# Performance work log

Measured on AMD Instinct MI355X. Metric: run time of the kernel, lower is better.

Reference implementation:

```python
import jax, jax.numpy as jnp
import numpy as np

# irreps '64x0e+32x1o+16x2e' as (mul, ir_dim, is_scalar)
IRREPS = [(64, 1, True), (32, 3, False), (16, 5, False)]
DIM = sum(m * d for m, d, _ in IRREPS)          # 240
NUM_FEATURES = sum(m for m, _, _ in IRREPS)      # 112
NUM_SCALAR = sum(m for m, _, s in IRREPS if s)   # 64
NUM_TYPE = 10
EPS = 1e-5
BATCH = 200000


def setup_inputs() -> dict:
    key = jax.random.key(0)
    k1, k2 = jax.random.split(key)
    x = jax.random.normal(k1, (BATCH, DIM), dtype=jnp.float32)
    input_type = jax.random.randint(k2, (BATCH,), 0, NUM_TYPE)
    weight = jnp.ones((NUM_TYPE, NUM_FEATURES), dtype=jnp.float32)
    bias = jnp.zeros((NUM_TYPE, NUM_SCALAR), dtype=jnp.float32)
    return {"x": x, "input_type": input_type, "weight": weight, "bias": bias}


def _type_mean(vals, input_type, counts):
    # scatter_mean over the batch dim into NUM_TYPE slots
    s = jax.ops.segment_sum(vals, input_type, num_segments=NUM_TYPE)
    return s / counts[:, None]


def reference(x, input_type, weight, bias):
    batch, dim = x.shape
    xr = x.reshape(batch, 1, dim)  # middle dim (no extra ... dims here)
    counts = jnp.maximum(
        jax.ops.segment_sum(jnp.ones((batch,), x.dtype), input_type, num_segments=NUM_TYPE),
        1.0,
    )
    fields = []
    ix = iw = ib = 0
    for mul, d, is_scalar in IRREPS:
        field = xr[:, :, ix:ix + mul * d].reshape(batch, -1, mul, d)
        ix += mul * d
        if is_scalar:
            fm = field.mean(1).reshape(batch, mul)                 # (batch, mul)
            fm = _type_mean(fm, input_type, counts)                # (num_type, mul)
            field = field - fm[input_type][:, None, :, None]
        # normalization='component': mean over ir dim; reduce='mean' over middle dim
        fn = jnp.square(field).mean(3).mean(1)                     # (batch, mul)
        fn = _type_mean(fn, input_type, counts)                    # (num_type, mul)
        fn = jax.lax.rsqrt(fn + EPS)
        fn = fn * weight[:, iw:iw + mul]
        iw += mul
        field = field * fn[input_type][:, None, :, None]
        if is_scalar:
            field = field + bias[:, ib:ib + mul][input_type][:, None, :, None]
            ib += mul
        fields.append(field.reshape(batch, -1, mul * d))
    out = jnp.concatenate(fields, axis=2)
    return out.reshape(batch, dim)
```

## Files before the change

### kernel.cpp

```cpp
#include <hip/hip_runtime.h>

#define DIM 240
#define NTYPE 10
#define NFEAT 112
#define NSLOT 176
#define NRED  1770
#define PSTRIDE 1792
#define RCHUNK 32
#define SROWS 16
#define EPSV 1e-5f

typedef float nf4 __attribute__((ext_vector_type(4)));


__global__ __launch_bounds__(256) void stats_kernel(const float* __restrict__ x,
        const int* __restrict__ type, float* __restrict__ partial, int B, int nblk)
{
    const int tid = threadIdx.x;
    const bool active = tid < DIM;
    const bool isScalar = tid < 64;

    float accA[NTYPE], accB[NTYPE];
#pragma unroll
    for (int t = 0; t < NTYPE; t++) { accA[t] = 0.f; accB[t] = 0.f; }

    const float inactAdd = (tid == 255) ? 1.f : 0.f;

    auto accum = [&](int ty, float v) {
        const float v2 = v * v;
        const float addA = active ? (isScalar ? v : v2) : inactAdd;
#pragma unroll
        for (int t = 0; t < NTYPE; t++) {
            if (t == ty) { accA[t] += addA; accB[t] += v2; }
        }
    };

    const int stride = nblk * SROWS;
    for (int row0 = blockIdx.x * SROWS; row0 + (SROWS - 1) < B; row0 += stride) {
        int ty[SROWS];
#pragma unroll
        for (int j = 0; j < SROWS; j++) ty[j] = type[row0 + j];
        float v[SROWS];
#pragma unroll
        for (int j = 0; j < SROWS; j++) v[j] = 0.f;
        if (active) {
            const float* p = x + (size_t)row0 * DIM + tid;
#pragma unroll
            for (int j = 0; j < SROWS; j++) v[j] = p[j * DIM];
        }
#pragma unroll
        for (int j = 0; j < SROWS; j++) accum(ty[j], v[j]);
    }
    if (blockIdx.x == 0) {
        for (int r = B & ~(SROWS - 1); r < B; r++) {
            const int ty0 = type[r];
            float v = active ? x[(size_t)r * DIM + tid] : 0.f;
            accum(ty0, v);
        }
    }

    __shared__ float sAcc[NRED];
    for (int i = tid; i < NRED; i += 256) sAcc[i] = 0.f;
    __syncthreads();

    if (isScalar) {
#pragma unroll
        for (int t = 0; t < NTYPE; t++) {
            sAcc[t * NSLOT + tid] = accA[t];
            sAcc[t * NSLOT + 64 + tid] = accB[t];
        }
    } else if (tid < 160) {
        const int ch = (tid - 64) / 3;
#pragma unroll
        for (int t = 0; t < NTYPE; t++)
            atomicAdd(&sAcc[t * NSLOT + 128 + ch], accA[t]);
    } else if (tid < DIM) {
        const int ch = (tid - 160) / 5;
#pragma unroll
        for (int t = 0; t < NTYPE; t++)
            atomicAdd(&sAcc[t * NSLOT + 160 + ch], accA[t]);
    } else if (tid == 255) {
#pragma unroll
        for (int t = 0; t < NTYPE; t++)
            sAcc[NTYPE * NSLOT + t] = accA[t];
    }
    __syncthreads();

    float* __restrict__ dst = partial + (size_t)blockIdx.x * PSTRIDE;
    for (int i = tid; i < NRED; i += 256) dst[i] = sAcc[i];
}

__global__ __launch_bounds__(256) void reduce1_kernel(const float* __restrict__ partial,
        float* __restrict__ gpart, int nblk)
{
    const int colChunk = blockIdx.x % 7;
    const int rowChunk = blockIdx.x / 7;
    const int col = colChunk * 256 + threadIdx.x;
    const int r0 = (rowChunk * nblk) / RCHUNK;
    const int r1 = ((rowChunk + 1) * nblk) / RCHUNK;
    float acc = 0.f;
#pragma unroll 8
    for (int r = r0; r < r1; r++)
        acc += partial[(size_t)r * PSTRIDE + col];
    gpart[rowChunk * PSTRIDE + col] = acc;
}

__global__ __launch_bounds__(256) void finalize_kernel(const float* __restrict__ gpart,
        const float* __restrict__ weight, const float* __restrict__ bias,
        float* __restrict__ params)
{
    const int t = blockIdx.x;
    const int c = threadIdx.x;

    __shared__ float scnt;
    if (c == 0) {
        float cs = 0.f;
#pragma unroll
        for (int k = 0; k < RCHUNK; k++)
            cs += gpart[k * PSTRIDE + NTYPE * NSLOT + t];
        scnt = fmaxf(cs, 1.f);
    }
    __syncthreads();
    if (c >= DIM) return;
    const float inv = 1.f / scnt;

    float sub = 0.f, mul, bia = 0.f;
    if (c < 64) {
        float S = 0.f, Q = 0.f;
#pragma unroll
        for (int k = 0; k < RCHUNK; k++) {
            const float* p = gpart + k * PSTRIDE + t * NSLOT;
            S += p[c]; Q += p[64 + c];
        }
        const float mean = S * inv;
        float var = Q * inv - mean * mean;
        var = fmaxf(var, 0.f);
        mul = rsqrtf(var + EPSV) * weight[t * NFEAT + c];
        sub = mean;
        bia = bias[t * 64 + c];
    } else if (c < 160) {
        const int ch = (c - 64) / 3;
        float N = 0.f;
#pragma unroll
        for (int k = 0; k < RCHUNK; k++)
            N += gpart[k * PSTRIDE + t * NSLOT + 128 + ch];
        mul = rsqrtf(N * inv * (1.f / 3.f) + EPSV) * weight[t * NFEAT + 64 + ch];
    } else {
        const int ch = (c - 160) / 5;
        float N = 0.f;
#pragma unroll
        for (int k = 0; k < RCHUNK; k++)
            N += gpart[k * PSTRIDE + t * NSLOT + 160 + ch];
        mul = rsqrtf(N * inv * 0.2f + EPSV) * weight[t * NFEAT + 96 + ch];
    }
    float* p = params + t * 720;
    p[c] = sub;
    p[240 + c] = mul;
    p[480 + c] = bia;
}

__global__ __launch_bounds__(256) void apply_kernel(const float* __restrict__ x,
        const int* __restrict__ type, const float* __restrict__ params,
        float* __restrict__ out, int B, int nblocks)
{
    __shared__ nf4 sp[NTYPE * 180];
    const int tid = threadIdx.x;
    const nf4* __restrict__ pg = (const nf4*)params;
    for (int i = tid; i < NTYPE * 180; i += 256) sp[i] = pg[i];
    __syncthreads();

    const int total = B * 60;
    const nf4* __restrict__ xv = (const nf4*)x;
    nf4* __restrict__ ov = (nf4*)out;
    const int estride = nblocks * 256;

    for (int base = blockIdx.x * 256 + tid; base < total; base += estride * 4) {
        int e0 = base, e1 = base + estride, e2 = base + 2 * estride, e3 = base + 3 * estride;
        const bool a0 = e0 < total, a1 = e1 < total, a2 = e2 < total, a3 = e3 < total;
        const int r0 = (int)(((unsigned long long)(unsigned)e0 * 2290649225ull) >> 37);
        const int r1 = a1 ? (int)(((unsigned long long)(unsigned)e1 * 2290649225ull) >> 37) : 0;
        const int r2 = a2 ? (int)(((unsigned long long)(unsigned)e2 * 2290649225ull) >> 37) : 0;
        const int r3 = a3 ? (int)(((unsigned long long)(unsigned)e3 * 2290649225ull) >> 37) : 0;
        const int c0 = e0 - r0 * 60, c1 = e1 - r1 * 60, c2 = e2 - r2 * 60, c3 = e3 - r3 * 60;
        int t0 = 0, t1 = 0, t2 = 0, t3 = 0;
        nf4 v0 = {0,0,0,0}, v1 = {0,0,0,0}, v2 = {0,0,0,0}, v3 = {0,0,0,0};
        if (a0) { t0 = type[r0]; v0 = xv[e0]; }
        if (a1) { t1 = type[r1]; v1 = xv[e1]; }
        if (a2) { t2 = type[r2]; v2 = xv[e2]; }
        if (a3) { t3 = type[r3]; v3 = xv[e3]; }
        if (a0) {
            const nf4 s = sp[t0 * 180 + c0];
            const nf4 m = sp[t0 * 180 + 60 + c0];
            const nf4 b = sp[t0 * 180 + 120 + c0];
            __builtin_nontemporal_store((v0 - s) * m + b, &ov[e0]);
        }
        if (a1) {
            const nf4 s = sp[t1 * 180 + c1];
            const nf4 m = sp[t1 * 180 + 60 + c1];
            const nf4 b = sp[t1 * 180 + 120 + c1];
            __builtin_nontemporal_store((v1 - s) * m + b, &ov[e1]);
        }
        if (a2) {
            const nf4 s = sp[t2 * 180 + c2];
            const nf4 m = sp[t2 * 180 + 60 + c2];
            const nf4 b = sp[t2 * 180 + 120 + c2];
            __builtin_nontemporal_store((v2 - s) * m + b, &ov[e2]);
        }
        if (a3) {
            const nf4 s = sp[t3 * 180 + c3];
            const nf4 m = sp[t3 * 180 + 60 + c3];
            const nf4 b = sp[t3 * 180 + 120 + c3];
            __builtin_nontemporal_store((v3 - s) * m + b, &ov[e3]);
        }
    }
}

extern "C" void kernel_launch(void* const* d_in, const int* in_sizes, int n_in,
                              void* d_out, int out_size, void* d_ws, size_t ws_size,
                              hipStream_t stream) {
    const float* x      = (const float*)d_in[0];
    const int*   type   = (const int*)d_in[1];
    const float* weight = (const float*)d_in[2];
    const float* bias   = (const float*)d_in[3];
    float* out = (float*)d_out;
    float* ws  = (float*)d_ws;
    const int B = in_sizes[0] / DIM;

    int nblk = 2048;
    size_t fixed = (size_t)RCHUNK * PSTRIDE + 7200;
    size_t need_floats = (size_t)nblk * PSTRIDE + fixed;
    if (ws_size < need_floats * 4) {
        nblk = (int)((ws_size / 4 - fixed) / PSTRIDE);
        if (nblk < 1) nblk = 1;
    }
    float* partial = ws;
    float* gpart   = ws + (size_t)nblk * PSTRIDE;
    float* params  = gpart + (size_t)RCHUNK * PSTRIDE;

    hipLaunchKernelGGL(stats_kernel, dim3(nblk), dim3(256), 0, stream,
                       x, type, partial, B, nblk);
    hipLaunchKernelGGL(reduce1_kernel, dim3(7 * RCHUNK), dim3(256), 0, stream,
                       partial, gpart, nblk);
    hipLaunchKernelGGL(finalize_kernel, dim3(NTYPE), dim3(256), 0, stream,
                       gpart, weight, bias, params);
    hipLaunchKernelGGL(apply_kernel, dim3(2048), dim3(256), 0, stream,
                       x, type, params, out, B, 2048);
}
```

Measured before the change: 379.9 us.

## Replace partial-sum reduction kernel with global atomics and compact apply params

The stats kernel now atomically adds each block's per-type sums into 32 striped global slots, zeroed by a memset beforehand. This removes the per-block partial buffer and the separate reduce1 kernel. The apply kernel's parameter table shrinks so that only the scalar channels load a mean and bias, while the other channels just multiply. In exchange, global atomics contend across 2048 blocks, a memset launch is added, and the summation order becomes nondeterministic.

```diff
diff --git a/kernel.cpp b/kernel.cpp
--- a/kernel.cpp
+++ b/kernel.cpp
@@ -8,13 +8,14 @@
 #define PSTRIDE 1792
 #define RCHUNK 32
 #define SROWS 16
+#define PT 384
 #define EPSV 1e-5f
 
 typedef float nf4 __attribute__((ext_vector_type(4)));
 
 
 __global__ __launch_bounds__(256) void stats_kernel(const float* __restrict__ x,
-        const int* __restrict__ type, float* __restrict__ partial, int B, int nblk)
+        const int* __restrict__ type, float* __restrict__ gpart, int B, int nblk)
 {
     const int tid = threadIdx.x;
     const bool active = tid < DIM;
@@ -86,23 +87,8 @@
     }
     __syncthreads();
 
-    float* __restrict__ dst = partial + (size_t)blockIdx.x * PSTRIDE;
-    for (int i = tid; i < NRED; i += 256) dst[i] = sAcc[i];
-}
-
-__global__ __launch_bounds__(256) void reduce1_kernel(const float* __restrict__ partial,
-        float* __restrict__ gpart, int nblk)
-{
-    const int colChunk = blockIdx.x % 7;
-    const int rowChunk = blockIdx.x / 7;
-    const int col = colChunk * 256 + threadIdx.x;
-    const int r0 = (rowChunk * nblk) / RCHUNK;
-    const int r1 = ((rowChunk + 1) * nblk) / RCHUNK;
-    float acc = 0.f;
-#pragma unroll 8
-    for (int r = r0; r < r1; r++)
-        acc += partial[(size_t)r * PSTRIDE + col];
-    gpart[rowChunk * PSTRIDE + col] = acc;
+    float* __restrict__ dst = gpart + (size_t)(blockIdx.x & (RCHUNK - 1)) * PSTRIDE;
+    for (int i = tid; i < NRED; i += 256) atomicAdd(&dst[i], sAcc[i]);
 }
 
 __global__ __launch_bounds__(256) void finalize_kernel(const float* __restrict__ gpart,
@@ -153,20 +139,19 @@
             N += gpart[k * PSTRIDE + t * NSLOT + 160 + ch];
         mul = rsqrtf(N * inv * 0.2f + EPSV) * weight[t * NFEAT + 96 + ch];
     }
-    float* p = params + t * 720;
-    p[c] = sub;
-    p[240 + c] = mul;
-    p[480 + c] = bia;
+    float* p = params + t * PT;
+    p[c] = mul;
+    if (c < 64) { p[240 + c] = sub; p[304 + c] = bia; }
 }
 
 __global__ __launch_bounds__(256) void apply_kernel(const float* __restrict__ x,
         const int* __restrict__ type, const float* __restrict__ params,
         float* __restrict__ out, int B, int nblocks)
 {
-    __shared__ nf4 sp[NTYPE * 180];
+    __shared__ nf4 sp[NTYPE * 96];
     const int tid = threadIdx.x;
     const nf4* __restrict__ pg = (const nf4*)params;
-    for (int i = tid; i < NTYPE * 180; i += 256) sp[i] = pg[i];
+    for (int i = tid; i < NTYPE * 96; i += 256) sp[i] = pg[i];
     __syncthreads();
 
     const int total = B * 60;
@@ -189,28 +174,28 @@
         if (a2) { t2 = type[r2]; v2 = xv[e2]; }
         if (a3) { t3 = type[r3]; v3 = xv[e3]; }
         if (a0) {
-            const nf4 s = sp[t0 * 180 + c0];
-            const nf4 m = sp[t0 * 180 + 60 + c0];
-            const nf4 b = sp[t0 * 180 + 120 + c0];
-            __builtin_nontemporal_store((v0 - s) * m + b, &ov[e0]);
+            const nf4 m = sp[t0 * 96 + c0];
+            nf4 o = v0 * m;
+            if (c0 < 16) o = (v0 - sp[t0 * 96 + 60 + c0]) * m + sp[t0 * 96 + 76 + c0];
+            __builtin_nontemporal_store(o, &ov[e0]);
         }
         if (a1) {
-            const nf4 s = sp[t1 * 180 + c1];
-            const nf4 m = sp[t1 * 180 + 60 + c1];
-            const nf4 b = sp[t1 * 180 + 120 + c1];
-            __builtin_nontemporal_store((v1 - s) * m + b, &ov[e1]);
+            const nf4 m = sp[t1 * 96 + c1];
+            nf4 o = v1 * m;
+            if (c1 < 16) o = (v1 - sp[t1 * 96 + 60 + c1]) * m + sp[t1 * 96 + 76 + c1];
+            __builtin_nontemporal_store(o, &ov[e1]);
         }
         if (a2) {
-            const nf4 s = sp[t2 * 180 + c2];
-            const nf4 m = sp[t2 * 180 + 60 + c2];
-            const nf4 b = sp[t2 * 180 + 120 + c2];
-            __builtin_nontemporal_store((v2 - s) * m + b, &ov[e2]);
+            const nf4 m = sp[t2 * 96 + c2];
+            nf4 o = v2 * m;
+            if (c2 < 16) o = (v2 - sp[t2 * 96 + 60 + c2]) * m + sp[t2 * 96 + 76 + c2];
+            __builtin_nontemporal_store(o, &ov[e2]);
         }
         if (a3) {
-            const nf4 s = sp[t3 * 180 + c3];
-            const nf4 m = sp[t3 * 180 + 60 + c3];
-            const nf4 b = sp[t3 * 180 + 120 + c3];
-            __builtin_nontemporal_store((v3 - s) * m + b, &ov[e3]);
+            const nf4 m = sp[t3 * 96 + c3];
+            nf4 o = v3 * m;
+            if (c3 < 16) o = (v3 - sp[t3 * 96 + 60 + c3]) * m + sp[t3 * 96 + 76 + c3];
+            __builtin_nontemporal_store(o, &ov[e3]);
         }
     }
 }
@@ -226,21 +211,12 @@
     float* ws  = (float*)d_ws;
     const int B = in_sizes[0] / DIM;
 
-    int nblk = 2048;
-    size_t fixed = (size_t)RCHUNK * PSTRIDE + 7200;
-    size_t need_floats = (size_t)nblk * PSTRIDE + fixed;
-    if (ws_size < need_floats * 4) {
-        nblk = (int)((ws_size / 4 - fixed) / PSTRIDE);
-        if (nblk < 1) nblk = 1;
-    }
-    float* partial = ws;
-    float* gpart   = ws + (size_t)nblk * PSTRIDE;
-    float* params  = gpart + (size_t)RCHUNK * PSTRIDE;
-
-    hipLaunchKernelGGL(stats_kernel, dim3(nblk), dim3(256), 0, stream,
-                       x, type, partial, B, nblk);
-    hipLaunchKernelGGL(reduce1_kernel, dim3(7 * RCHUNK), dim3(256), 0, stream,
-                       partial, gpart, nblk);
+    float* gpart  = ws;
+    float* params = ws + (size_t)RCHUNK * PSTRIDE;
+
+    hipMemsetAsync(gpart, 0, (size_t)RCHUNK * PSTRIDE * sizeof(float), stream);
+    hipLaunchKernelGGL(stats_kernel, dim3(2048), dim3(256), 0, stream,
+                       x, type, gpart, B, 2048);
     hipLaunchKernelGGL(finalize_kernel, dim3(NTYPE), dim3(256), 0, stream,
                        gpart, weight, bias, params);
     hipLaunchKernelGGL(apply_kernel, dim3(2048), dim3(256), 0, stream,
```

Result: faster. 370.9 us (-2.4%).
